# Optimization experiments

Hardware: AMD Instinct MI355X
Metric: run time of the kernel (lower is better)

The kernel has to match this reference:

```python
import math
import jax, jax.numpy as jnp
import numpy as np

B, N, D, NH, DFF, DRAW, TMAX = 4, 1024, 512, 8, 2048, 32, 2
DK = D // NH
LN_EPS = 1e-5


def bayes_linear(x, w_mu, w_rho, b_mu, b_rho):
    # closed-form mean/variance of a variational linear layer
    w_sig = jax.nn.softplus(w_rho)
    b_sig = jax.nn.softplus(b_rho)
    mean = x @ w_mu.T + b_mu
    var = (x * x) @ (w_sig * w_sig).T + b_sig * b_sig
    return mean, var


def layer_norm(x, g, b):
    mu = jnp.mean(x, axis=-1, keepdims=True)
    v = jnp.var(x, axis=-1, keepdims=True)
    return (x - mu) / jnp.sqrt(v + LN_EPS) * g + b


def gelu_deriv(x):
    phi = 0.5 * (1.0 + jax.lax.erf(x / math.sqrt(2.0)))
    pdf = jnp.exp(-0.5 * x * x) / math.sqrt(2.0 * math.pi)
    return phi + x * pdf


def attention(x, x_raw, w_mu, w_rho, b_mu, b_rho, log_sigma_f, log_length):
    Bb, Nn, Dd = x.shape
    qm, _ = bayes_linear(x, w_mu[0], w_rho[0], b_mu[0], b_rho[0])
    km, _ = bayes_linear(x, w_mu[1], w_rho[1], b_mu[1], b_rho[1])
    vm, vv = bayes_linear(x, w_mu[2], w_rho[2], b_mu[2], b_rho[2])

    def heads(t):
        return t.reshape(Bb, Nn, NH, DK).transpose(0, 2, 1, 3)  # [B,H,N,dk]

    Q, K, V, Vv = heads(qm), heads(km), heads(vm), heads(vv)
    scores = jnp.einsum('bhnd,bhmd->bhnm', Q, K) / math.sqrt(DK)
    # RBF kernel on raw inputs, per head; dist2 via |x|^2+|x'|^2-2xx' (no [B,N,N,d] diff tensor)
    sq = jnp.sum(x_raw * x_raw, axis=-1)
    dist2 = jnp.maximum(sq[:, :, None] + sq[:, None, :] - 2.0 * jnp.einsum('bnd,bmd->bnm', x_raw, x_raw), 0.0)
    sigma_f2 = jnp.exp(2.0 * log_sigma_f)
    length2 = jnp.exp(2.0 * log_length)
    rbf = sigma_f2[None, :, None, None] * jnp.exp(-dist2[:, None, :, :] / (2.0 * length2[None, :, None, None]))
    attn = jax.nn.softmax(scores + rbf, axis=-1)
    ctx = jnp.einsum('bhnm,bhmd->bhnd', attn, V).transpose(0, 2, 1, 3).reshape(Bb, Nn, Dd)
    vta = jnp.einsum('bhnm,bhmd->bhnd', attn * attn, Vv).transpose(0, 2, 1, 3).reshape(Bb, Nn, Dd)
    om, ovp = bayes_linear(ctx, w_mu[3], w_rho[3], b_mu[3], b_rho[3])
    return om, ovp + vta


def ffn(x, w1_mu, w1_rho, b1_mu, b1_rho, w2_mu, w2_rho, b2_mu, b2_rho):
    hm, hv = bayes_linear(x, w1_mu, w1_rho, b1_mu, b1_rho)
    am = jax.nn.gelu(hm, approximate=False)
    av = gelu_deriv(hm) ** 2 * hv
    om, ovd = bayes_linear(am, w2_mu, w2_rho, b2_mu, b2_rho)
    w2_sig = jax.nn.softplus(w2_rho)
    vc = av @ (w2_mu * w2_mu + w2_sig * w2_sig).T
    return om, ovd + vc


def cascade(H, H_var, tau_k, x_raw, attn_w_mu, attn_w_rho, attn_b_mu, attn_b_rho,
            w1_mu, w1_rho, b1_mu, b1_rho, w2_mu, w2_rho, b2_mu, b2_rho,
            ln1_g, ln1_b, ln2_g, ln2_b, log_sigma_f, log_length, log_gammas):
    g = jax.nn.softplus(log_gammas)
    g1, g2, g3, g4 = g[0], g[1], g[2], g[3]
    alpha = g1 / (g1 + g2)  # E[alpha] (inference path)
    beta = g3 / (g3 + g4)
    Va = g1 * g2 / ((g1 + g2) ** 2 * (g1 + g2 + 1.0))
    Vb = g3 * g4 / ((g3 + g4) ** 2 * (g3 + g4 + 1.0))
    done = jnp.asarray(False)
    for _ in range(TMAX):
        n1 = layer_norm(H, ln1_g, ln1_b)
        am, avar = attention(n1, x_raw, attn_w_mu, attn_w_rho, attn_b_mu, attn_b_rho, log_sigma_f, log_length)
        Hb = H + am
        n2 = layer_norm(Hb, ln2_g, ln2_b)
        fm, fvar = ffn(n2, w1_mu, w1_rho, b1_mu, b1_rho, w2_mu, w2_rho, b2_mu, b2_rho)
        F_out = Hb + fm
        F_var = avar + fvar
        Hn = alpha * H + beta * F_out
        Hvn = (alpha ** 2) * H_var + (beta ** 2) * F_var + Va * H * H + Vb * F_out * F_out + Va * H_var + Vb * F_var
        H = jnp.where(done, H, Hn)
        H_var = jnp.where(done, H_var, Hvn)
        done = done | (jnp.mean(H_var) <= tau_k)  # early-exit freeze
    return H, H_var


def setup_inputs() -> dict:
    key = jax.random.key(0)
    ks = jax.random.split(key, 8)
    inp = {
        'H': jax.random.normal(ks[0], (B, N, D), jnp.float32),
        'H_var': jax.random.uniform(ks[1], (B, N, D), jnp.float32) * 0.1,
        'x_raw': jax.random.normal(ks[2], (B, N, DRAW), jnp.float32) * 0.15,
        'tau_k': jnp.zeros((), jnp.float32),
        'attn_w_mu': jax.random.normal(ks[3], (4, D, D), jnp.float32) / math.sqrt(D),
        'attn_w_rho': jnp.full((4, D, D), -3.0, jnp.float32),
        'attn_b_mu': jnp.zeros((4, D), jnp.float32),
        'attn_b_rho': jnp.full((4, D), -3.0, jnp.float32),
        'w1_mu': jax.random.normal(ks[4], (DFF, D), jnp.float32) / math.sqrt(D),
        'w1_rho': jnp.full((DFF, D), -3.0, jnp.float32),
        'b1_mu': jnp.zeros((DFF,), jnp.float32),
        'b1_rho': jnp.full((DFF,), -3.0, jnp.float32),
        'w2_mu': jax.random.normal(ks[5], (D, DFF), jnp.float32) / math.sqrt(DFF),
        'w2_rho': jnp.full((D, DFF), -3.0, jnp.float32),
        'b2_mu': jnp.zeros((D,), jnp.float32),
        'b2_rho': jnp.full((D,), -3.0, jnp.float32),
        'ln1_g': jnp.ones((D,), jnp.float32),
        'ln1_b': jnp.zeros((D,), jnp.float32),
        'ln2_g': jnp.ones((D,), jnp.float32),
        'ln2_b': jnp.zeros((D,), jnp.float32),
        'log_sigma_f': jnp.zeros((NH,), jnp.float32),
        'log_length': jnp.zeros((NH,), jnp.float32),
        'log_gammas': jnp.ones((4,), jnp.float32),
    }
    return inp


def reference(H, H_var, x_raw, tau_k, attn_w_mu, attn_w_rho, attn_b_mu, attn_b_rho,
              w1_mu, w1_rho, b1_mu, b1_rho, w2_mu, w2_rho, b2_mu, b2_rho,
              ln1_g, ln1_b, ln2_g, ln2_b, log_sigma_f, log_length, log_gammas):
    return cascade(H, H_var, tau_k, x_raw, attn_w_mu, attn_w_rho, attn_b_mu, attn_b_rho,
                   w1_mu, w1_rho, b1_mu, b1_rho, w2_mu, w2_rho, b2_mu, b2_rho,
                   ln1_g, ln1_b, ln2_g, ln2_b, log_sigma_f, log_length, log_gammas)
```

## Files before the change

### kernel.cpp

```cpp
#include <hip/hip_runtime.h>
#include <math.h>


#define Bx   4
#define Nx   1024
#define Dx   512
#define NHx  8
#define DFFx 2048

static constexpr size_t BN  = (size_t)Bx * Nx;
static constexpr size_t BND = BN * Dx;
static constexpr size_t BNF = BN * DFFx;
static constexpr int    DD  = Dx * Dx;
static constexpr int    DF  = DFFx * Dx;

typedef __attribute__((ext_vector_type(8))) short bf16x8;
typedef __attribute__((ext_vector_type(4))) float f32x4;

__device__ __forceinline__ float sp_(float x) {
  return x > 20.f ? x : log1pf(expf(x));
}
__device__ __forceinline__ unsigned short f2b(float f) {
  unsigned u = __float_as_uint(f);
  unsigned r = (u + 0x7fffu + ((u >> 16) & 1u)) >> 16;
  return (unsigned short)r;
}
__device__ __forceinline__ float b2f(unsigned short v) {
  return __uint_as_float((unsigned)v << 16);
}

__global__ __launch_bounds__(256) void cvt_weights(
    const float* __restrict__ aw_mu, const float* __restrict__ aw_rho,
    const float* __restrict__ w1_mu, const float* __restrict__ w1_rho,
    const float* __restrict__ w2_mu, const float* __restrict__ w2_rho,
    const float* __restrict__ attn_b_rho, const float* __restrict__ b1_rho,
    const float* __restrict__ b2_rho, const float* __restrict__ xraw,
    unsigned short* __restrict__ aw_bf,
    unsigned short* __restrict__ wvvar_bf,
    unsigned short* __restrict__ wovar_bf,
    unsigned short* __restrict__ w1_bf, unsigned short* __restrict__ w1var_bf,
    unsigned short* __restrict__ w2_bf, unsigned short* __restrict__ w2var_bf,
    unsigned short* __restrict__ w2comb_bf,
    float* __restrict__ bv2, float* __restrict__ bo2,
    float* __restrict__ b1v, float* __restrict__ b2v,
    float* __restrict__ sqb)
{
  int i = blockIdx.x * 256 + threadIdx.x;
  if (i < 4 * DD) {
    aw_bf[i] = f2b(aw_mu[i]);
  } else if (i < 6 * DD) {
    int j = i - 4 * DD;
    if (j < DD) { float s = sp_(aw_rho[2 * DD + j]); wvvar_bf[j] = f2b(s * s); }
    else { int k = j - DD; float s = sp_(aw_rho[3 * DD + k]); wovar_bf[k] = f2b(s * s); }
  } else if (i < 6 * DD + DF) {
    int j = i - 6 * DD;
    w1_bf[j] = f2b(w1_mu[j]);
  } else if (i < 6 * DD + 2 * DF) {
    int j = i - 6 * DD - DF;
    float s = sp_(w1_rho[j]); w1var_bf[j] = f2b(s * s);
  } else if (i < 6 * DD + 3 * DF) {
    int j = i - 6 * DD - 2 * DF;
    float m = w2_mu[j];
    float s = sp_(w2_rho[j]); float v = s * s;
    w2_bf[j] = f2b(m);
    w2var_bf[j] = f2b(v);
    w2comb_bf[j] = f2b(m * m + v);
  } else {
    int j = i - (6 * DD + 3 * DF);
    if (j < 512) {
      float s = sp_(attn_b_rho[1024 + j]); bv2[j] = s * s;
    } else if (j < 1024) {
      int k = j - 512;
      float s = sp_(attn_b_rho[1536 + k]); bo2[k] = s * s;
    } else if (j < 3072) {
      int k = j - 1024;
      float s = sp_(b1_rho[k]); b1v[k] = s * s;
    } else if (j < 3584) {
      int k = j - 3072;
      float s = sp_(b2_rho[k]); b2v[k] = s * s;
    } else if (j < 3584 + (int)BN) {
      int row = j - 3584;
      const float* x = xraw + (size_t)row * 32;
      float acc = 0.f;
      #pragma unroll
      for (int t = 0; t < 32; t++) acc += x[t] * x[t];
      sqb[row] = acc;
    }
  }
}

__global__ __launch_bounds__(256) void gram_rbf(
    const float* __restrict__ xraw, const float* __restrict__ sqb,
    const float* __restrict__ lsf, const float* __restrict__ lll,
    unsigned short* __restrict__ rbf)
{
  const int nt = blockIdx.x, mt = blockIdx.y, b = blockIdx.z;
  __shared__ float xn[64][36];
  __shared__ float xm[64][36];
  __shared__ float sn[64], sm[64];
  const int tid = threadIdx.x;
  for (int q = tid; q < 512; q += 256) {
    int rr = q >> 3, cc = (q & 7) << 2;
    *(float4*)&xn[rr][cc] =
        *(const float4*)(xraw + ((size_t)b * Nx + nt * 64 + rr) * 32 + cc);
    *(float4*)&xm[rr][cc] =
        *(const float4*)(xraw + ((size_t)b * Nx + mt * 64 + rr) * 32 + cc);
  }
  if (tid < 64) {
    sn[tid] = sqb[(size_t)b * Nx + nt * 64 + tid];
    sm[tid] = sqb[(size_t)b * Nx + mt * 64 + tid];
  }
  __syncthreads();
  const int r = tid >> 2, j = tid & 3;
  float dd[16];
  #pragma unroll
  for (int i = 0; i < 16; i++) {
    int mm = j * 16 + i;
    float g = 0.f;
    #pragma unroll
    for (int t = 0; t < 32; t++) g += xn[r][t] * xm[mm][t];
    dd[i] = fmaxf(sn[r] + sm[mm] - 2.f * g, 0.f);
  }
  const int n = nt * 64 + r;
  #pragma unroll
  for (int h = 0; h < NHx; h++) {
    float sf2 = expf(2.f * lsf[h]);
    float i2l = 0.5f * expf(-2.f * lll[h]);
    unsigned short tmp[16];
    #pragma unroll
    for (int i = 0; i < 16; i++) tmp[i] = f2b(sf2 * expf(-dd[i] * i2l));
    unsigned short* dst =
        rbf + ((size_t)(h * Bx + b) * Nx + n) * Nx + mt * 64 + j * 16;
    *(uint4*)dst = *(const uint4*)&tmp[0];
    *(uint4*)(dst + 8) = *(const uint4*)&tmp[8];
  }
}

__global__ __launch_bounds__(256) void layernorm_bf(
    const float* __restrict__ X, const float* __restrict__ g,
    const float* __restrict__ bta,
    unsigned short* __restrict__ Y, unsigned short* __restrict__ Ysq)
{
  const int row = blockIdx.x;
  const float* x = X + (size_t)row * Dx;
  const int tid = threadIdx.x;
  float v0 = x[tid], v1 = x[tid + 256];
  float s = v0 + v1;
  float ss = v0 * v0 + v1 * v1;
  #pragma unroll
  for (int o = 32; o > 0; o >>= 1) {
    s += __shfl_down(s, o);
    ss += __shfl_down(ss, o);
  }
  __shared__ float ps[4], pss[4];
  const int w = tid >> 6;
  if ((tid & 63) == 0) { ps[w] = s; pss[w] = ss; }
  __syncthreads();
  float S = ps[0] + ps[1] + ps[2] + ps[3];
  float SS = pss[0] + pss[1] + pss[2] + pss[3];
  float mean = S * (1.f / 512.f);
  float var = fmaxf(SS * (1.f / 512.f) - mean * mean, 0.f);
  float inv = rsqrtf(var + 1e-5f);
  float y0 = (v0 - mean) * inv * g[tid] + bta[tid];
  float y1 = (v1 - mean) * inv * g[tid + 256] + bta[tid + 256];
  Y[(size_t)row * Dx + tid] = f2b(y0);
  Y[(size_t)row * Dx + tid + 256] = f2b(y1);
  Ysq[(size_t)row * Dx + tid] = f2b(y0 * y0);
  Ysq[(size_t)row * Dx + tid + 256] = f2b(y1 * y1);
}

struct GD {
  const unsigned short* A;
  const unsigned short* W;
  const float* bias;
  const float* add_in;
  void* C;
  int N;
  int trans;
};

template <bool HALFM, bool OUTBF>
__global__ __launch_bounds__(256) void gemm_mf(
    GD d0, GD d1, GD d2, int M, int K, int ldc)
{
  const GD d = (blockIdx.z == 0) ? d0 : ((blockIdx.z == 1) ? d1 : d2);
  const int n0 = blockIdx.x * 128;
  if (n0 >= d.N) return;
  constexpr int BM = HALFM ? 64 : 128;
  const int m0 = blockIdx.y * BM;

  __shared__ short As0[BM * 32];
  __shared__ short As1[BM * 32];
  __shared__ short Ws0[128 * 32];
  __shared__ short Ws1[128 * 32];

  const int tid = threadIdx.x;
  const int lane = tid & 63;
  const int wv = tid >> 6;
  const int wr = wv >> 1, wc = wv & 1;
  const int fr = lane & 15;
  const int fk = (lane >> 4) * 8;

  const int rowA = m0 + (tid >> 2);
  const int rowW = n0 + (tid >> 2);
  const int colc = (tid & 3) * 8;
  const unsigned short* gA0 = d.A + (size_t)rowA * K + colc;
  const unsigned short* gA1 = gA0 + (size_t)64 * K;
  const unsigned short* gW0 = d.W + (size_t)rowW * K + colc;
  const unsigned short* gW1 = gW0 + (size_t)64 * K;
  short* lA00 = &As0[tid * 8];
  short* lA01 = &As1[tid * 8];
  short* lA10 = &As0[(tid + 256) * 8];
  short* lA11 = &As1[(tid + 256) * 8];
  short* lW00 = &Ws0[tid * 8];
  short* lW01 = &Ws1[tid * 8];
  short* lW10 = &Ws0[(tid + 256) * 8];
  short* lW11 = &Ws1[(tid + 256) * 8];

  constexpr int MI = BM / 32;
  f32x4 acc[MI][4] = {};

  uint4 ra0, ra1, ra2, ra3, rw0, rw1, rw2, rw3;
  {
    ra0 = *(const uint4*)(gA0);
    ra1 = *(const uint4*)(gA0 + 32);
    if (!HALFM) {
      ra2 = *(const uint4*)(gA1);
      ra3 = *(const uint4*)(gA1 + 32);
    }
    rw0 = *(const uint4*)(gW0);
    rw1 = *(const uint4*)(gW0 + 32);
    rw2 = *(const uint4*)(gW1);
    rw3 = *(const uint4*)(gW1 + 32);
  }

  for (int k0 = 0; k0 < K; k0 += 64) {
    __syncthreads();
    *(uint4*)lA00 = ra0;
    *(uint4*)lA01 = ra1;
    if (!HALFM) {
      *(uint4*)lA10 = ra2;
      *(uint4*)lA11 = ra3;
    }
    *(uint4*)lW00 = rw0;
    *(uint4*)lW01 = rw1;
    *(uint4*)lW10 = rw2;
    *(uint4*)lW11 = rw3;
    __syncthreads();

    if (k0 + 64 < K) {
      int kn = k0 + 64;
      ra0 = *(const uint4*)(gA0 + kn);
      ra1 = *(const uint4*)(gA0 + kn + 32);
      if (!HALFM) {
        ra2 = *(const uint4*)(gA1 + kn);
        ra3 = *(const uint4*)(gA1 + kn + 32);
      }
      rw0 = *(const uint4*)(gW0 + kn);
      rw1 = *(const uint4*)(gW0 + kn + 32);
      rw2 = *(const uint4*)(gW1 + kn);
      rw3 = *(const uint4*)(gW1 + kn + 32);
    }

    {
      bf16x8 af[MI], bfr[4];
      #pragma unroll
      for (int mi = 0; mi < MI; mi++)
        af[mi] = *(const bf16x8*)&As0[(wr * (BM / 2) + mi * 16 + fr) * 32 + fk];
      #pragma unroll
      for (int ni = 0; ni < 4; ni++)
        bfr[ni] = *(const bf16x8*)&Ws0[(wc * 64 + ni * 16 + fr) * 32 + fk];
      #pragma unroll
      for (int mi = 0; mi < MI; mi++)
        #pragma unroll
        for (int ni = 0; ni < 4; ni++)
          acc[mi][ni] = __builtin_amdgcn_mfma_f32_16x16x32_bf16(
              af[mi], bfr[ni], acc[mi][ni], 0, 0, 0);
    }
    {
      bf16x8 af[MI], bfr[4];
      #pragma unroll
      for (int mi = 0; mi < MI; mi++)
        af[mi] = *(const bf16x8*)&As1[(wr * (BM / 2) + mi * 16 + fr) * 32 + fk];
      #pragma unroll
      for (int ni = 0; ni < 4; ni++)
        bfr[ni] = *(const bf16x8*)&Ws1[(wc * 64 + ni * 16 + fr) * 32 + fk];
      #pragma unroll
      for (int mi = 0; mi < MI; mi++)
        #pragma unroll
        for (int ni = 0; ni < 4; ni++)
          acc[mi][ni] = __builtin_amdgcn_mfma_f32_16x16x32_bf16(
              af[mi], bfr[ni], acc[mi][ni], 0, 0, 0);
    }
  }

  const int quad = lane >> 4;
  #pragma unroll
  for (int mi = 0; mi < MI; mi++) {
    #pragma unroll
    for (int ni = 0; ni < 4; ni++) {
      int col = n0 + wc * 64 + ni * 16 + fr;
      if (col >= d.N) continue;
      float bv = d.bias ? d.bias[col] : 0.f;
      int rowb = m0 + wr * (BM / 2) + mi * 16 + quad * 4;
      if (d.trans) {
        ushort4 o;
        o.x = f2b(acc[mi][ni][0] + bv);
        o.y = f2b(acc[mi][ni][1] + bv);
        o.z = f2b(acc[mi][ni][2] + bv);
        o.w = f2b(acc[mi][ni][3] + bv);
        *(ushort4*)&((unsigned short*)d.C)[(size_t)col * M + rowb] = o;
      } else {
        #pragma unroll
        for (int r = 0; r < 4; r++) {
          float v = acc[mi][ni][r] + bv;
          if (d.add_in) v += d.add_in[(size_t)(rowb + r) * ldc + col];
          if (OUTBF)
            ((unsigned short*)d.C)[(size_t)(rowb + r) * ldc + col] = f2b(v);
          else
            ((float*)d.C)[(size_t)(rowb + r) * ldc + col] = v;
        }
      }
    }
  }
}

__global__ __launch_bounds__(256) void flash_mfma(
    const unsigned short* __restrict__ QK,
    const unsigned short* __restrict__ VT,
    const unsigned short* __restrict__ rbf,
    unsigned short* __restrict__ ctx_bf, unsigned short* __restrict__ ctxsq_bf,
    float* __restrict__ vta)
{
  const int qt = blockIdx.x, h = blockIdx.y, b = blockIdx.z;
  const int q0 = qt * 64;
  const int tid = threadIdx.x;
  const int w = tid >> 6;
  const int lane = tid & 63;
  const int fr = lane & 15;
  const int quad = lane >> 4;

  __shared__ unsigned short Kt[64 * 72];
  __shared__ unsigned short VtT[64 * 72];
  __shared__ unsigned short VvT[64 * 72];
  __shared__ unsigned short Pt[64 * 72];
  __shared__ unsigned short P2t[64 * 72];
  __shared__ float lred[4][16];

  bf16x8 qa0, qa1;
  {
    const unsigned short* qp =
        QK + ((size_t)(b * Nx + q0 + w * 16 + fr)) * 1024 + h * 64 + quad * 8;
    qa0 = *(const bf16x8*)qp;
    qa1 = *(const bf16x8*)(qp + 32);
  }

  float lsum[4] = {0.f, 0.f, 0.f, 0.f};
  f32x4 accO[4] = {};
  f32x4 accW[4] = {};

  const unsigned short* kg = QK + ((size_t)b * Nx) * 1024 + 512 + h * 64;
  const unsigned short* vg = VT + (size_t)(h * 64) * BN + b * Nx;
  const unsigned short* ug = VT + (size_t)(512 + h * 64) * BN + b * Nx;
  const unsigned short* rb =
      rbf + ((size_t)(h * Bx + b) * Nx + q0 + w * 16 + quad * 4) * Nx;

  const int a0 = tid >> 3;
  const int c8 = (tid & 7) * 8;

  uint4 pk0, pk1, pv0, pv1, pu0, pu1;
  pk0 = *(const uint4*)(kg + (size_t)a0 * 1024 + c8);
  pk1 = *(const uint4*)(kg + (size_t)(a0 + 32) * 1024 + c8);
  pv0 = *(const uint4*)(vg + (size_t)a0 * BN + c8);
  pv1 = *(const uint4*)(vg + (size_t)(a0 + 32) * BN + c8);
  pu0 = *(const uint4*)(ug + (size_t)a0 * BN + c8);
  pu1 = *(const uint4*)(ug + (size_t)(a0 + 32) * BN + c8);

  for (int mt = 0; mt < 16; mt++) {
    __syncthreads();
    *(uint4*)&Kt[a0 * 72 + c8] = pk0;
    *(uint4*)&Kt[(a0 + 32) * 72 + c8] = pk1;
    *(uint4*)&VtT[a0 * 72 + c8] = pv0;
    *(uint4*)&VtT[(a0 + 32) * 72 + c8] = pv1;
    *(uint4*)&VvT[a0 * 72 + c8] = pu0;
    *(uint4*)&VvT[(a0 + 32) * 72 + c8] = pu1;
    __syncthreads();

    if (mt + 1 < 16) {
      const int n1 = (mt + 1) * 64;
      pk0 = *(const uint4*)(kg + (size_t)(n1 + a0) * 1024 + c8);
      pk1 = *(const uint4*)(kg + (size_t)(n1 + a0 + 32) * 1024 + c8);
      pv0 = *(const uint4*)(vg + (size_t)a0 * BN + n1 + c8);
      pv1 = *(const uint4*)(vg + (size_t)(a0 + 32) * BN + n1 + c8);
      pu0 = *(const uint4*)(ug + (size_t)a0 * BN + n1 + c8);
      pu1 = *(const uint4*)(ug + (size_t)(a0 + 32) * BN + n1 + c8);
    }

    f32x4 accS[4] = {};
    #pragma unroll
    for (int ni = 0; ni < 4; ni++) {
      bf16x8 b0 = *(const bf16x8*)&Kt[(ni * 16 + fr) * 72 + quad * 8];
      bf16x8 b1 = *(const bf16x8*)&Kt[(ni * 16 + fr) * 72 + 32 + quad * 8];
      accS[ni] = __builtin_amdgcn_mfma_f32_16x16x32_bf16(qa0, b0, accS[ni], 0, 0, 0);
      accS[ni] = __builtin_amdgcn_mfma_f32_16x16x32_bf16(qa1, b1, accS[ni], 0, 0, 0);
    }

    const int m0 = mt * 64;
    #pragma unroll
    for (int reg = 0; reg < 4; reg++) {
      const unsigned short* rr = rb + (size_t)reg * Nx + m0;
      int rowb = (w * 16 + quad * 4 + reg) * 72;
      #pragma unroll
      for (int ni = 0; ni < 4; ni++) {
        float pv = expf(accS[ni][reg] * 0.125f + b2f(rr[ni * 16 + fr]));
        lsum[reg] += pv;
        Pt[rowb + ni * 16 + fr] = f2b(pv);
        P2t[rowb + ni * 16 + fr] = f2b(pv * pv);
      }
    }
    __syncthreads();

    #pragma unroll
    for (int ks = 0; ks < 2; ks++) {
      bf16x8 pa  = *(const bf16x8*)&Pt[(w * 16 + fr) * 72 + ks * 32 + quad * 8];
      bf16x8 p2a = *(const bf16x8*)&P2t[(w * 16 + fr) * 72 + ks * 32 + quad * 8];
      #pragma unroll
      for (int ni = 0; ni < 4; ni++) {
        bf16x8 vb = *(const bf16x8*)&VtT[(ni * 16 + fr) * 72 + ks * 32 + quad * 8];
        bf16x8 ub = *(const bf16x8*)&VvT[(ni * 16 + fr) * 72 + ks * 32 + quad * 8];
        accO[ni] = __builtin_amdgcn_mfma_f32_16x16x32_bf16(vb, pa, accO[ni], 0, 0, 0);
        accW[ni] = __builtin_amdgcn_mfma_f32_16x16x32_bf16(ub, p2a, accW[ni], 0, 0, 0);
      }
    }
  }

  #pragma unroll
  for (int reg = 0; reg < 4; reg++) {
    float t = lsum[reg];
    t += __shfl_xor(t, 1);
    t += __shfl_xor(t, 2);
    t += __shfl_xor(t, 4);
    t += __shfl_xor(t, 8);
    lsum[reg] = t;
  }
  if (fr == 0) {
    #pragma unroll
    for (int reg = 0; reg < 4; reg++) lred[w][quad * 4 + reg] = lsum[reg];
  }
  __syncthreads();
  float invl = 1.f / lred[w][fr];
  float invl2 = invl * invl;

  size_t row = (size_t)b * Nx + q0 + w * 16 + fr;
  #pragma unroll
  for (int ni = 0; ni < 4; ni++) {
    int dkb = h * 64 + ni * 16 + quad * 4;
    ushort4 oc, oc2;
    float4 ov;
    float c0 = accO[ni][0] * invl, c1 = accO[ni][1] * invl;
    float c2 = accO[ni][2] * invl, c3 = accO[ni][3] * invl;
    oc.x = f2b(c0); oc.y = f2b(c1); oc.z = f2b(c2); oc.w = f2b(c3);
    oc2.x = f2b(c0 * c0); oc2.y = f2b(c1 * c1);
    oc2.z = f2b(c2 * c2); oc2.w = f2b(c3 * c3);
    ov.x = accW[ni][0] * invl2; ov.y = accW[ni][1] * invl2;
    ov.z = accW[ni][2] * invl2; ov.w = accW[ni][3] * invl2;
    *(ushort4*)&ctx_bf[row * Dx + dkb] = oc;
    *(ushort4*)&ctxsq_bf[row * Dx + dkb] = oc2;
    *(float4*)&vta[row * Dx + dkb] = ov;
  }
}

__global__ __launch_bounds__(256) void gelu_triple(
    unsigned short* __restrict__ hm, unsigned short* __restrict__ hv,
    unsigned short* __restrict__ am2)
{
  size_t i8 = ((size_t)blockIdx.x * 256 + threadIdx.x) * 8;
  uint4 hm8 = *(const uint4*)&hm[i8];
  uint4 hv8 = *(const uint4*)&hv[i8];
  const unsigned short* ms = (const unsigned short*)&hm8;
  const unsigned short* vs = (const unsigned short*)&hv8;
  unsigned short oa[8], ob[8], oc[8];
  #pragma unroll
  for (int j = 0; j < 8; j++) {
    float x = b2f(ms[j]);
    float phi = 0.5f * (1.f + erff(x * 0.70710678118654752f));
    float pdf = expf(-0.5f * x * x) * 0.39894228040143268f;
    float am = x * phi;
    float gd = phi + x * pdf;
    oa[j] = f2b(am);
    ob[j] = f2b(am * am);
    oc[j] = f2b(gd * gd * b2f(vs[j]));
  }
  *(uint4*)&hm[i8] = *(const uint4*)&oa[0];
  *(uint4*)&am2[i8] = *(const uint4*)&ob[0];
  *(uint4*)&hv[i8] = *(const uint4*)&oc[0];
}

__global__ __launch_bounds__(256) void combine_k(
    const float* __restrict__ Hin, const float* __restrict__ Hvin,
    float* __restrict__ Hout, float* __restrict__ Hvout,
    const float* __restrict__ F, const float* __restrict__ fva,
    const float* __restrict__ vc, const float* __restrict__ lg)
{
  size_t i = ((size_t)blockIdx.x * 256 + threadIdx.x) * 4;
  float g1 = sp_(lg[0]), g2 = sp_(lg[1]), g3 = sp_(lg[2]), g4 = sp_(lg[3]);
  float s12 = g1 + g2, s34 = g3 + g4;
  float alpha = g1 / s12, beta = g3 / s34;
  float Va = g1 * g2 / (s12 * s12 * (s12 + 1.f));
  float Vb = g3 * g4 / (s34 * s34 * (s34 + 1.f));
  float4 h4 = *(const float4*)&Hin[i];
  float4 hv4 = *(const float4*)&Hvin[i];
  float4 F4 = *(const float4*)&F[i];
  float4 a4 = *(const float4*)&fva[i];
  float4 c4 = *(const float4*)&vc[i];
  float* hp = (float*)&h4; float* vp = (float*)&hv4;
  const float* Fp = (const float*)&F4; const float* ap = (const float*)&a4;
  const float* cp = (const float*)&c4;
  float4 ho, vo;
  float* hop = (float*)&ho; float* vop = (float*)&vo;
  #pragma unroll
  for (int j = 0; j < 4; j++) {
    float h = hp[j], hv = vp[j];
    float Fm = Fp[j];
    float Fv = ap[j] + cp[j];
    hop[j] = alpha * h + beta * Fm;
    vop[j] = alpha * alpha * hv + beta * beta * Fv + Va * h * h + Vb * Fm * Fm +
             Va * hv + Vb * Fv;
  }
  *(float4*)&Hout[i] = ho;
  *(float4*)&Hvout[i] = vo;
}

extern "C" void kernel_launch(void* const* d_in, const int* in_sizes, int n_in,
                              void* d_out, int out_size, void* d_ws, size_t ws_size,
                              hipStream_t stream)
{
  const float* H_in   = (const float*)d_in[0];
  const float* Hv_in  = (const float*)d_in[1];
  const float* x_raw  = (const float*)d_in[2];
  const float* aw_mu  = (const float*)d_in[4];
  const float* aw_rho = (const float*)d_in[5];
  const float* ab_mu  = (const float*)d_in[6];
  const float* ab_rho = (const float*)d_in[7];
  const float* w1_mu  = (const float*)d_in[8];
  const float* w1_rho = (const float*)d_in[9];
  const float* b1_mu  = (const float*)d_in[10];
  const float* b1_rho = (const float*)d_in[11];
  const float* w2_mu  = (const float*)d_in[12];
  const float* w2_rho = (const float*)d_in[13];
  const float* b2_mu  = (const float*)d_in[14];
  const float* b2_rho = (const float*)d_in[15];
  const float* ln1_g  = (const float*)d_in[16];
  const float* ln1_b  = (const float*)d_in[17];
  const float* ln2_g  = (const float*)d_in[18];
  const float* ln2_b  = (const float*)d_in[19];
  const float* lsf    = (const float*)d_in[20];
  const float* lll    = (const float*)d_in[21];
  const float* lgam   = (const float*)d_in[22];

  float* Hout = (float*)d_out;
  float* Hvar = (float*)d_out + BND;

  float* ws = (float*)d_ws;
  size_t off = 0;
  auto allocf = [&](size_t n) {
    float* p = ws + off; off += (n + 7) & ~(size_t)7; return p;
  };
  auto allocus = [&](size_t n) {
    return (unsigned short*)allocf((n + 1) / 2);
  };
  unsigned short* rbf = allocus((size_t)NHx * Bx * Nx * Nx);
  float* vta = allocf(BND);
  float* Hb  = allocf(BND);
  float* fva = allocf(BND);
  float* vc  = allocf(BND);
  unsigned short* QKb = allocus(BN * 1024);
  unsigned short* VTb = allocus((size_t)1024 * BN);
  unsigned short* lnA = allocus(BND);
  unsigned short* lnB = allocus(BND);
  unsigned short* hm_bf  = allocus(BNF);
  unsigned short* hv_bf  = allocus(BNF);
  unsigned short* am2_bf = allocus(BNF);
  unsigned short* aw_bf     = allocus(4 * DD);
  unsigned short* wvvar_bf  = allocus(DD);
  unsigned short* wovar_bf  = allocus(DD);
  unsigned short* w1_bf     = allocus(DF);
  unsigned short* w1var_bf  = allocus(DF);
  unsigned short* w2_bf     = allocus(DF);
  unsigned short* w2var_bf  = allocus(DF);
  unsigned short* w2comb_bf = allocus(DF);
  float* bv2 = allocf(512);
  float* bo2 = allocf(512);
  float* b1v = allocf(2048);
  float* b2v = allocf(512);
  float* sqb = allocf(BN);
  (void)ws_size; (void)in_sizes; (void)n_in; (void)out_size;

  {
    int tot = 6 * DD + 3 * DF + 3584 + (int)BN;
    cvt_weights<<<(tot + 255) / 256, 256, 0, stream>>>(
        aw_mu, aw_rho, w1_mu, w1_rho, w2_mu, w2_rho,
        ab_rho, b1_rho, b2_rho, x_raw,
        aw_bf, wvvar_bf, wovar_bf, w1_bf, w1var_bf, w2_bf, w2var_bf,
        w2comb_bf, bv2, bo2, b1v, b2v, sqb);
  }
  gram_rbf<<<dim3(16, 16, Bx), 256, 0, stream>>>(x_raw, sqb, lsf, lll, rbf);

  const int M = (int)BN;
  GD dz = {nullptr, nullptr, nullptr, nullptr, nullptr, 0, 0};

  const float* Hsrc  = H_in;
  const float* Hvsrc = Hv_in;

  for (int t = 0; t < 2; t++) {
    layernorm_bf<<<(int)BN, 256, 0, stream>>>(Hsrc, ln1_g, ln1_b, lnA, lnB);
    {
      GD dqk = {lnA, aw_bf, ab_mu, nullptr, (void*)QKb, 1024, 0};
      GD dv  = {lnA, aw_bf + 2 * (size_t)DD, ab_mu + 1024, nullptr,
                (void*)VTb, 512, 1};
      GD dvv = {lnB, wvvar_bf, bv2, nullptr,
                (void*)(VTb + (size_t)512 * BN), 512, 1};
      gemm_mf<false, true><<<dim3(8, 32, 3), 256, 0, stream>>>(
          dqk, dv, dvv, M, 512, 1024);
    }
    flash_mfma<<<dim3(Nx / 64, NHx, Bx), 256, 0, stream>>>(
        QKb, VTb, rbf, lnA, lnB, vta);
    {
      GD d_om = {lnA, aw_bf + 3 * (size_t)DD, ab_mu + 1536, Hsrc, (void*)Hb,
                 512, 0};
      GD d_ov = {lnB, wovar_bf, bo2, vta, (void*)vta, 512, 0};
      gemm_mf<true, false><<<dim3(4, 64, 2), 256, 0, stream>>>(
          d_om, d_ov, dz, M, 512, 512);
    }

    layernorm_bf<<<(int)BN, 256, 0, stream>>>(Hb, ln2_g, ln2_b, lnA, lnB);
    {
      GD d_hm = {lnA, w1_bf, b1_mu, nullptr, (void*)hm_bf, 2048, 0};
      GD d_hv = {lnB, w1var_bf, b1v, nullptr, (void*)hv_bf, 2048, 0};
      gemm_mf<false, true><<<dim3(16, 32, 2), 256, 0, stream>>>(
          d_hm, d_hv, dz, M, 512, 2048);
    }
    gelu_triple<<<(int)(BNF / (256 * 8)), 256, 0, stream>>>(hm_bf, hv_bf, am2_bf);
    {
      GD d_fm  = {hm_bf, w2_bf, b2_mu, Hb, (void*)Hb, 512, 0};
      GD d_ovd = {am2_bf, w2var_bf, b2v, vta, (void*)fva, 512, 0};
      GD d_vc  = {hv_bf, w2comb_bf, nullptr, nullptr, (void*)vc, 512, 0};
      gemm_mf<true, false><<<dim3(4, 64, 3), 256, 0, stream>>>(
          d_fm, d_ovd, d_vc, M, 2048, 512);
    }
    combine_k<<<(int)(BND / (256 * 4)), 256, 0, stream>>>(
        Hsrc, Hvsrc, Hout, Hvar, Hb, fva, vc, lgam);

    Hsrc = Hout;
    Hvsrc = Hvar;
  }
}
```

Before: 594.5 us.

## Fuse FFN1 mean/variance GEMMs with GELU epilogue; use fast exp; rotate RBF smem index

Adds a dedicated gemm_ffn1 kernel that computes both the FFN1 mean and variance GEMMs in one block and applies the GELU mean/variance epilogue directly. This removes the separate gelu_triple pass and the round trip of hm/hv through global memory. It also switches expf to __expf in the RBF and flash-attention kernels, and rotates the inner-product index in the RBF kernel to avoid LDS bank conflicts. The risks are slightly lower exp accuracy and a new GEMM whose tiling and epilogue stores (scalar 2-byte writes) may be less efficient than the generic one.

New measurement: 636.6 us. +7.1%, slower.

```diff
diff --git a/kernel.cpp b/kernel.cpp
--- a/kernel.cpp
+++ b/kernel.cpp
@@ -118,17 +118,20 @@
     int mm = j * 16 + i;
     float g = 0.f;
     #pragma unroll
-    for (int t = 0; t < 32; t++) g += xn[r][t] * xm[mm][t];
+    for (int t = 0; t < 32; t++) {
+      int tt = (t + mm) & 31;
+      g += xn[r][tt] * xm[mm][tt];
+    }
     dd[i] = fmaxf(sn[r] + sm[mm] - 2.f * g, 0.f);
   }
   const int n = nt * 64 + r;
   #pragma unroll
   for (int h = 0; h < NHx; h++) {
-    float sf2 = expf(2.f * lsf[h]);
-    float i2l = 0.5f * expf(-2.f * lll[h]);
+    float sf2 = __expf(2.f * lsf[h]);
+    float i2l = 0.5f * __expf(-2.f * lll[h]);
     unsigned short tmp[16];
     #pragma unroll
-    for (int i = 0; i < 16; i++) tmp[i] = f2b(sf2 * expf(-dd[i] * i2l));
+    for (int i = 0; i < 16; i++) tmp[i] = f2b(sf2 * __expf(-dd[i] * i2l));
     unsigned short* dst =
         rbf + ((size_t)(h * Bx + b) * Nx + n) * Nx + mt * 64 + j * 16;
     *(uint4*)dst = *(const uint4*)&tmp[0];
@@ -325,6 +328,124 @@
   }
 }
 
+__global__ __launch_bounds__(256) void gemm_ffn1(
+    const unsigned short* __restrict__ A1, const unsigned short* __restrict__ A2,
+    const unsigned short* __restrict__ W1, const unsigned short* __restrict__ W2,
+    const float* __restrict__ b1, const float* __restrict__ b2,
+    unsigned short* __restrict__ am_o, unsigned short* __restrict__ am2_o,
+    unsigned short* __restrict__ av_o)
+{
+  const int n0 = blockIdx.x * 128;
+  const int m0 = blockIdx.y * 64;
+  constexpr int K = 512;
+
+  __shared__ short As0[64 * 32], As1[64 * 32];
+  __shared__ short Bs0[64 * 32], Bs1[64 * 32];
+  __shared__ short Ws0[128 * 32], Ws1[128 * 32];
+  __shared__ short Vs0[128 * 32], Vs1[128 * 32];
+
+  const int tid = threadIdx.x;
+  const int lane = tid & 63;
+  const int wv = tid >> 6;
+  const int wr = wv >> 1, wc = wv & 1;
+  const int fr = lane & 15;
+  const int fk = (lane >> 4) * 8;
+
+  const int rowA = m0 + (tid >> 2);
+  const int rowW = n0 + (tid >> 2);
+  const int colc = (tid & 3) * 8;
+  const unsigned short* gA1 = A1 + (size_t)rowA * K + colc;
+  const unsigned short* gA2 = A2 + (size_t)rowA * K + colc;
+  const unsigned short* gW1a = W1 + (size_t)rowW * K + colc;
+  const unsigned short* gW1b = gW1a + (size_t)64 * K;
+  const unsigned short* gW2a = W2 + (size_t)rowW * K + colc;
+  const unsigned short* gW2b = gW2a + (size_t)64 * K;
+
+  f32x4 accA[2][4] = {};
+  f32x4 accB[2][4] = {};
+
+  uint4 ra0, ra1, rb0, rb1, rw0, rw1, rw2, rw3, rv0, rv1, rv2, rv3;
+  ra0 = *(const uint4*)(gA1);      ra1 = *(const uint4*)(gA1 + 32);
+  rb0 = *(const uint4*)(gA2);      rb1 = *(const uint4*)(gA2 + 32);
+  rw0 = *(const uint4*)(gW1a);     rw1 = *(const uint4*)(gW1a + 32);
+  rw2 = *(const uint4*)(gW1b);     rw3 = *(const uint4*)(gW1b + 32);
+  rv0 = *(const uint4*)(gW2a);     rv1 = *(const uint4*)(gW2a + 32);
+  rv2 = *(const uint4*)(gW2b);     rv3 = *(const uint4*)(gW2b + 32);
+
+  for (int k0 = 0; k0 < K; k0 += 64) {
+    __syncthreads();
+    *(uint4*)&As0[tid * 8] = ra0;  *(uint4*)&As1[tid * 8] = ra1;
+    *(uint4*)&Bs0[tid * 8] = rb0;  *(uint4*)&Bs1[tid * 8] = rb1;
+    *(uint4*)&Ws0[tid * 8] = rw0;  *(uint4*)&Ws1[tid * 8] = rw1;
+    *(uint4*)&Ws0[(tid + 256) * 8] = rw2;  *(uint4*)&Ws1[(tid + 256) * 8] = rw3;
+    *(uint4*)&Vs0[tid * 8] = rv0;  *(uint4*)&Vs1[tid * 8] = rv1;
+    *(uint4*)&Vs0[(tid + 256) * 8] = rv2;  *(uint4*)&Vs1[(tid + 256) * 8] = rv3;
+    __syncthreads();
+
+    if (k0 + 64 < K) {
+      int kn = k0 + 64;
+      ra0 = *(const uint4*)(gA1 + kn);  ra1 = *(const uint4*)(gA1 + kn + 32);
+      rb0 = *(const uint4*)(gA2 + kn);  rb1 = *(const uint4*)(gA2 + kn + 32);
+      rw0 = *(const uint4*)(gW1a + kn); rw1 = *(const uint4*)(gW1a + kn + 32);
+      rw2 = *(const uint4*)(gW1b + kn); rw3 = *(const uint4*)(gW1b + kn + 32);
+      rv0 = *(const uint4*)(gW2a + kn); rv1 = *(const uint4*)(gW2a + kn + 32);
+      rv2 = *(const uint4*)(gW2b + kn); rv3 = *(const uint4*)(gW2b + kn + 32);
+    }
+
+    #pragma unroll
+    for (int half = 0; half < 2; half++) {
+      const short* As = half ? As1 : As0;
+      const short* Bs = half ? Bs1 : Bs0;
+      const short* Ws = half ? Ws1 : Ws0;
+      const short* Vs = half ? Vs1 : Vs0;
+      bf16x8 afA[2], afB[2], wf[4], vf[4];
+      #pragma unroll
+      for (int mi = 0; mi < 2; mi++) {
+        afA[mi] = *(const bf16x8*)&As[(wr * 32 + mi * 16 + fr) * 32 + fk];
+        afB[mi] = *(const bf16x8*)&Bs[(wr * 32 + mi * 16 + fr) * 32 + fk];
+      }
+      #pragma unroll
+      for (int ni = 0; ni < 4; ni++) {
+        wf[ni] = *(const bf16x8*)&Ws[(wc * 64 + ni * 16 + fr) * 32 + fk];
+        vf[ni] = *(const bf16x8*)&Vs[(wc * 64 + ni * 16 + fr) * 32 + fk];
+      }
+      #pragma unroll
+      for (int mi = 0; mi < 2; mi++)
+        #pragma unroll
+        for (int ni = 0; ni < 4; ni++) {
+          accA[mi][ni] = __builtin_amdgcn_mfma_f32_16x16x32_bf16(
+              afA[mi], wf[ni], accA[mi][ni], 0, 0, 0);
+          accB[mi][ni] = __builtin_amdgcn_mfma_f32_16x16x32_bf16(
+              afB[mi], vf[ni], accB[mi][ni], 0, 0, 0);
+        }
+    }
+  }
+
+  const int quad = lane >> 4;
+  #pragma unroll
+  for (int mi = 0; mi < 2; mi++) {
+    #pragma unroll
+    for (int ni = 0; ni < 4; ni++) {
+      int col = n0 + wc * 64 + ni * 16 + fr;
+      float bb1 = b1[col], bb2 = b2[col];
+      int rowb = m0 + wr * 32 + mi * 16 + quad * 4;
+      #pragma unroll
+      for (int r = 0; r < 4; r++) {
+        float hm = accA[mi][ni][r] + bb1;
+        float hv = accB[mi][ni][r] + bb2;
+        float phi = 0.5f * (1.f + erff(hm * 0.70710678118654752f));
+        float pdf = __expf(-0.5f * hm * hm) * 0.39894228040143268f;
+        float am = hm * phi;
+        float gd = phi + hm * pdf;
+        size_t idx = (size_t)(rowb + r) * DFFx + col;
+        am_o[idx] = f2b(am);
+        am2_o[idx] = f2b(am * am);
+        av_o[idx] = f2b(gd * gd * hv);
+      }
+    }
+  }
+}
+
 __global__ __launch_bounds__(256) void flash_mfma(
     const unsigned short* __restrict__ QK,
     const unsigned short* __restrict__ VT,
@@ -412,7 +533,7 @@
       int rowb = (w * 16 + quad * 4 + reg) * 72;
       #pragma unroll
       for (int ni = 0; ni < 4; ni++) {
-        float pv = expf(accS[ni][reg] * 0.125f + b2f(rr[ni * 16 + fr]));
+        float pv = __expf(accS[ni][reg] * 0.125f + b2f(rr[ni * 16 + fr]));
         lsum[reg] += pv;
         Pt[rowb + ni * 16 + fr] = f2b(pv);
         P2t[rowb + ni * 16 + fr] = f2b(pv * pv);
@@ -468,32 +589,6 @@
     *(ushort4*)&ctxsq_bf[row * Dx + dkb] = oc2;
     *(float4*)&vta[row * Dx + dkb] = ov;
   }
-}
-
-__global__ __launch_bounds__(256) void gelu_triple(
-    unsigned short* __restrict__ hm, unsigned short* __restrict__ hv,
-    unsigned short* __restrict__ am2)
-{
-  size_t i8 = ((size_t)blockIdx.x * 256 + threadIdx.x) * 8;
-  uint4 hm8 = *(const uint4*)&hm[i8];
-  uint4 hv8 = *(const uint4*)&hv[i8];
-  const unsigned short* ms = (const unsigned short*)&hm8;
-  const unsigned short* vs = (const unsigned short*)&hv8;
-  unsigned short oa[8], ob[8], oc[8];
-  #pragma unroll
-  for (int j = 0; j < 8; j++) {
-    float x = b2f(ms[j]);
-    float phi = 0.5f * (1.f + erff(x * 0.70710678118654752f));
-    float pdf = expf(-0.5f * x * x) * 0.39894228040143268f;
-    float am = x * phi;
-    float gd = phi + x * pdf;
-    oa[j] = f2b(am);
-    ob[j] = f2b(am * am);
-    oc[j] = f2b(gd * gd * b2f(vs[j]));
-  }
-  *(uint4*)&hm[i8] = *(const uint4*)&oa[0];
-  *(uint4*)&am2[i8] = *(const uint4*)&ob[0];
-  *(uint4*)&hv[i8] = *(const uint4*)&oc[0];
 }
 
 __global__ __launch_bounds__(256) void combine_k(
@@ -578,9 +673,9 @@
   unsigned short* VTb = allocus((size_t)1024 * BN);
   unsigned short* lnA = allocus(BND);
   unsigned short* lnB = allocus(BND);
-  unsigned short* hm_bf  = allocus(BNF);
-  unsigned short* hv_bf  = allocus(BNF);
+  unsigned short* am_bf  = allocus(BNF);
   unsigned short* am2_bf = allocus(BNF);
+  unsigned short* av_bf  = allocus(BNF);
   unsigned short* aw_bf     = allocus(4 * DD);
   unsigned short* wvvar_bf  = allocus(DD);
   unsigned short* wovar_bf  = allocus(DD);
@@ -634,17 +729,12 @@
     }
 
     layernorm_bf<<<(int)BN, 256, 0, stream>>>(Hb, ln2_g, ln2_b, lnA, lnB);
+    gemm_ffn1<<<dim3(16, 64), 256, 0, stream>>>(
+        lnA, lnB, w1_bf, w1var_bf, b1_mu, b1v, am_bf, am2_bf, av_bf);
     {
-      GD d_hm = {lnA, w1_bf, b1_mu, nullptr, (void*)hm_bf, 2048, 0};
-      GD d_hv = {lnB, w1var_bf, b1v, nullptr, (void*)hv_bf, 2048, 0};
-      gemm_mf<false, true><<<dim3(16, 32, 2), 256, 0, stream>>>(
-          d_hm, d_hv, dz, M, 512, 2048);
-    }
-    gelu_triple<<<(int)(BNF / (256 * 8)), 256, 0, stream>>>(hm_bf, hv_bf, am2_bf);
-    {
-      GD d_fm  = {hm_bf, w2_bf, b2_mu, Hb, (void*)Hb, 512, 0};
+      GD d_fm  = {am_bf, w2_bf, b2_mu, Hb, (void*)Hb, 512, 0};
       GD d_ovd = {am2_bf, w2var_bf, b2v, vta, (void*)fva, 512, 0};
-      GD d_vc  = {hv_bf, w2comb_bf, nullptr, nullptr, (void*)vc, 512, 0};
+      GD d_vc  = {av_bf, w2comb_bf, nullptr, nullptr, (void*)vc, 512, 0};
       gemm_mf<true, false><<<dim3(4, 64, 3), 256, 0, stream>>>(
           d_fm, d_ovd, d_vc, M, 2048, 512);
     }
```
